# Performance work log

Measured on AMD Instinct MI355X. Metric: run time of the kernel, lower is better.

## Reference

```python
import jax, jax.numpy as jnp
import numpy as np

D_MODEL = 1024
NUM_HEADS = 16
D_K = D_MODEL // NUM_HEADS


def setup_inputs() -> dict:
    key = jax.random.key(0)
    ks = jax.random.split(key, 9)
    B, S = 4, 2048
    s = 1.0 / np.sqrt(D_MODEL)
    return {
        "x": jax.random.normal(ks[0], (B, S, D_MODEL), dtype=jnp.float32),
        "Wq": jax.random.uniform(ks[1], (D_MODEL, D_MODEL), jnp.float32, -s, s),
        "bq": jax.random.uniform(ks[2], (D_MODEL,), jnp.float32, -s, s),
        "Wk": jax.random.uniform(ks[3], (D_MODEL, D_MODEL), jnp.float32, -s, s),
        "bk": jax.random.uniform(ks[4], (D_MODEL,), jnp.float32, -s, s),
        "Wv": jax.random.uniform(ks[5], (D_MODEL, D_MODEL), jnp.float32, -s, s),
        "bv": jax.random.uniform(ks[6], (D_MODEL,), jnp.float32, -s, s),
        "Wo": jax.random.uniform(ks[7], (D_MODEL, D_MODEL), jnp.float32, -s, s),
        "bo": jax.random.uniform(ks[8], (D_MODEL,), jnp.float32, -s, s),
    }


def reference(x, Wq, bq, Wk, bk, Wv, bv, Wo, bo):
    B, S, D = x.shape
    H, dk = NUM_HEADS, D_K

    def proj(W, b):
        # [B,S,D] -> [B,H,S,dk]  (torch Linear: x @ W^T + b)
        y = jnp.einsum('bsd,ed->bse', x, W) + b
        return y.reshape(B, S, H, dk).transpose(0, 2, 1, 3)

    Q = proj(Wq, bq)
    K = proj(Wk, bk)
    V = proj(Wv, bv)

    scale = 1.0 / jnp.sqrt(jnp.asarray(dk, x.dtype))
    scores = jnp.einsum('bhqd,bhkd->bhqk', Q, K) * scale  # [B,H,S,S]
    attn = jax.nn.softmax(scores, axis=-1)
    # dropout is identity in eval mode
    out = jnp.einsum('bhqk,bhkd->bhqd', attn, V)  # [B,H,S,dk]
    out = out.transpose(0, 2, 1, 3).reshape(B, S, D)
    return jnp.einsum('bsd,ed->bse', out, Wo) + bo
```

## Files before the change

kernel.cpp:

```cpp
#include <hip/hip_runtime.h>


typedef unsigned short u16;
typedef unsigned int u32;
typedef __attribute__((ext_vector_type(8))) short bf16x8;
typedef __attribute__((ext_vector_type(4))) float f32x4;
typedef __attribute__((ext_vector_type(4))) unsigned short u16x4;
typedef __attribute__((ext_vector_type(8))) unsigned short u16x8;

#define SEQ    2048
#define DMODEL 1024
#define NHEAD  16
#define DK     64
#define BATCH  4
#define MROWS  (BATCH * SEQ)
#define LCF    0.18033688011112042f

__device__ __forceinline__ u16 f2bf(float f) {
  unsigned int u = __float_as_uint(f);
  u += 0x7fffu + ((u >> 16) & 1u);
  return (u16)(u >> 16);
}

__device__ __forceinline__ void gload_lds16(const void* g, void* l) {
  __builtin_amdgcn_global_load_lds((const __attribute__((address_space(1))) void*)g,
                                   (__attribute__((address_space(3))) void*)l,
                                   16, 0, 0);
}

__global__ __launch_bounds__(256) void cvt_all(const float* __restrict__ x,
                                               const float* __restrict__ w0,
                                               const float* __restrict__ w1,
                                               const float* __restrict__ w2,
                                               const float* __restrict__ w3,
                                               u16* xb, u16* o0, u16* o1, u16* o2, u16* o3) {
  const int NX4 = MROWS * DMODEL / 4;
  int i = blockIdx.x * 256 + threadIdx.x;
  const float* src; u16* dst; int off;
  if (i < NX4) { src = x; dst = xb; off = i; }
  else {
    int j = i - NX4;
    int wi = j >> 18; off = j & 0x3FFFF;
    src = wi == 0 ? w0 : wi == 1 ? w1 : wi == 2 ? w2 : w3;
    dst = wi == 0 ? o0 : wi == 1 ? o1 : wi == 2 ? o2 : o3;
  }
  float4 v = ((const float4*)src)[off];
  u16x4 o;
  o.x = f2bf(v.x); o.y = f2bf(v.y); o.z = f2bf(v.z); o.w = f2bf(v.w);
  ((u16x4*)dst)[off] = o;
}

__global__ __launch_bounds__(256) void vtrans(const u16* __restrict__ vb,
                                              u16* __restrict__ vt) {
  __shared__ u16 T[64 * 80];
  const int t = threadIdx.x;
  const int st = blockIdx.x;
  const int bh = blockIdx.y;
  const int b = bh >> 4, h = bh & 15;
  const size_t ibase = (size_t)b * SEQ * DMODEL + h * DK + (size_t)st * 64 * DMODEL;
#pragma unroll
  for (int i = 0; i < 2; ++i) {
    const int r = (t >> 3) + i * 32, c = (t & 7) * 8;
    *(bf16x8*)&T[r * 80 + c] = *(const bf16x8*)(vb + ibase + (size_t)r * DMODEL + c);
  }
  __syncthreads();
  const int d = t >> 2, k0 = (t & 3) * 16;
  const size_t obase = (((size_t)bh) * DK + d) * SEQ + st * 64 + k0;
  u16x8 a, bv;
#pragma unroll
  for (int j = 0; j < 8; ++j) a[j]  = T[(k0 + j) * 80 + d];
#pragma unroll
  for (int j = 0; j < 8; ++j) bv[j] = T[(k0 + 8 + j) * 80 + d];
  *(u16x8*)(vt + obase)     = a;
  *(u16x8*)(vt + obase + 8) = bv;
}

template <int OUT_BF16>
__device__ __forceinline__ void gemm_body(const u16* __restrict__ A,
                                          const u16* __restrict__ Bw,
                                          const float* __restrict__ bias,
                                          void* __restrict__ outp,
                                          int bm, int bn, int M, int N, int K,
                                          float scale, u16* As, u16* Bs) {
  const int t = threadIdx.x, w = t >> 6, l = t & 63;
  const int wr = (w >> 1) * 64, wc = (w & 1) * 64;
  const int lrow = l & 15, kgrp = l >> 4;
  const int r_in = l >> 3;
  const int c_in = ((l & 7) ^ r_in) * 8;
  const int sw = lrow & 7;

  f32x4 acc[4][4] = {};

  for (int kt = 0; kt < K; kt += 64) {
#pragma unroll
    for (int it = 0; it < 4; ++it) {
      const int chunk = w * 4 + it;
      const int row = chunk * 8 + r_in;
      gload_lds16(A  + (size_t)(bm * 128 + row) * K + kt + c_in, (char*)As + chunk * 1024);
      gload_lds16(Bw + (size_t)(bn * 128 + row) * K + kt + c_in, (char*)Bs + chunk * 1024);
    }
    __syncthreads();
#pragma unroll
    for (int kc = 0; kc < 2; ++kc) {
      bf16x8 af[4], bfr[4];
      const int slot = (kc * 4 + kgrp) ^ sw;
#pragma unroll
      for (int m = 0; m < 4; ++m)
        af[m] = *(const bf16x8*)&As[(wr + m * 16 + lrow) * 64 + slot * 8];
#pragma unroll
      for (int n = 0; n < 4; ++n)
        bfr[n] = *(const bf16x8*)&Bs[(wc + n * 16 + lrow) * 64 + slot * 8];
#pragma unroll
      for (int m = 0; m < 4; ++m)
#pragma unroll
        for (int n = 0; n < 4; ++n)
          acc[m][n] = __builtin_amdgcn_mfma_f32_16x16x32_bf16(af[m], bfr[n], acc[m][n], 0, 0, 0);
    }
    __syncthreads();
  }

  const int cr0 = bm * 128 + wr, cc0 = bn * 128 + wc;
#pragma unroll
  for (int n = 0; n < 4; ++n) {
    const int col = cc0 + n * 16 + lrow;
    const float bv = bias[col];
#pragma unroll
    for (int m = 0; m < 4; ++m) {
#pragma unroll
      for (int r = 0; r < 4; ++r) {
        const int row = cr0 + m * 16 + kgrp * 4 + r;
        const float v = (acc[m][n][r] + bv) * scale;
        if (OUT_BF16) ((u16*)outp)[(size_t)row * N + col] = f2bf(v);
        else          ((float*)outp)[(size_t)row * N + col] = v;
      }
    }
  }
}

__global__ __launch_bounds__(256) void gemm_bt_f32(const u16* __restrict__ A,
                                                   const u16* __restrict__ Bw,
                                                   const float* __restrict__ bias,
                                                   float* __restrict__ outp,
                                                   int M, int N, int K) {
  __shared__ u16 As[128 * 64];
  __shared__ u16 Bs[128 * 64];
  gemm_body<0>(A, Bw, bias, outp, blockIdx.x, blockIdx.y, M, N, K, 1.0f, As, Bs);
}

__global__ __launch_bounds__(256) void gemm_qkv(const u16* __restrict__ A,
                                                const u16* __restrict__ W0,
                                                const u16* __restrict__ W1,
                                                const u16* __restrict__ W2,
                                                const float* __restrict__ b0,
                                                const float* __restrict__ b1,
                                                const float* __restrict__ b2,
                                                u16* o0, u16* o1, u16* o2) {
  __shared__ u16 As[128 * 64];
  __shared__ u16 Bs[128 * 64];
  const int sel = blockIdx.y >> 3, bn = blockIdx.y & 7;
  const u16* Bw = sel == 0 ? W0 : sel == 1 ? W1 : W2;
  const float* bias = sel == 0 ? b0 : sel == 1 ? b1 : b2;
  u16* outp = sel == 0 ? o0 : sel == 1 ? o1 : o2;
  const float scale = sel == 0 ? LCF : 1.0f;
  gemm_body<1>(A, Bw, bias, outp, blockIdx.x, bn, MROWS, DMODEL, DMODEL, scale, As, Bs);
}

__global__ __launch_bounds__(256, 4) void attn_kernel(const u16* __restrict__ Qg,
                                                      const u16* __restrict__ Kg,
                                                      const u16* __restrict__ Vt,
                                                      u16* __restrict__ Og) {
  __shared__ u16 Ks[2][64 * 64];
  __shared__ u16 Vs[2][64 * 64];

  const int t = threadIdx.x, w = t >> 6, l = t & 63;
  const int lrow = l & 15, kgrp = l >> 4;
  const int sw = lrow & 7;

  const int id = blockIdx.x;
  const int swzid = (id & 7) * 128 + (id >> 3);
  const int qt = swzid & 15, bh = swzid >> 4;
  const int b = bh >> 4, h = bh & 15;
  const size_t base  = (size_t)b * SEQ * DMODEL + h * DK;
  const size_t vbase = (size_t)bh * DK * SEQ;
  const int r_in = l >> 3;
  const int c_in = ((l & 7) ^ r_in) * 8;

  int kro[2];
#pragma unroll
  for (int it = 0; it < 2; ++it) {
    const int p = (w * 2 + it) * 8 + r_in;
    const int n_ = p >> 4, g_ = (p >> 2) & 3, rr = p & 3;
    kro[it] = (n_ >> 1) * 32 + g_ * 8 + (n_ & 1) * 4 + rr;
  }

  const int qr = qt * 128 + w * 32;
  bf16x8 aq[2][2];
#pragma unroll
  for (int rg = 0; rg < 2; ++rg) {
    const u16* qp = Qg + base + (size_t)(qr + rg * 16 + lrow) * DMODEL + kgrp * 8;
    aq[rg][0] = *(const bf16x8*)qp;
    aq[rg][1] = *(const bf16x8*)(qp + 32);
  }

  f32x4 o_acc[2][4] = {};
  float lsum[2] = {};

#define STAGE(kt_, buf_)                                                        \
  {                                                                             \
    const int k0_ = (kt_) * 64;                                                 \
    _Pragma("unroll")                                                           \
    for (int it = 0; it < 2; ++it) {                                            \
      const int chunk = w * 2 + it;                                             \
      const int r = chunk * 8 + r_in;                                           \
      gload_lds16(Kg + base + (size_t)(k0_ + kro[it]) * DMODEL + c_in,          \
                  (char*)&Ks[buf_][0] + chunk * 1024);                          \
      gload_lds16(Vt + vbase + (size_t)r * SEQ + k0_ + c_in,                    \
                  (char*)&Vs[buf_][0] + chunk * 1024);                          \
    }                                                                           \
  }

  STAGE(0, 0);

  for (int kt = 0; kt < SEQ / 64; ++kt) {
    const int buf = kt & 1;
    __syncthreads();
    if (kt + 1 < SEQ / 64) STAGE(kt + 1, buf ^ 1);

    f32x4 sc[2][4] = {};
    __builtin_amdgcn_s_setprio(1);
#pragma unroll
    for (int kc = 0; kc < 2; ++kc) {
      const int slot = (kc * 4 + kgrp) ^ sw;
#pragma unroll
      for (int n = 0; n < 4; ++n) {
        bf16x8 bk = *(const bf16x8*)&Ks[buf][(n * 16 + lrow) * 64 + slot * 8];
        sc[0][n] = __builtin_amdgcn_mfma_f32_16x16x32_bf16(bk, aq[0][kc], sc[0][n], 0, 0, 0);
        sc[1][n] = __builtin_amdgcn_mfma_f32_16x16x32_bf16(bk, aq[1][kc], sc[1][n], 0, 0, 0);
      }
    }
    __builtin_amdgcn_s_setprio(0);

    bf16x8 pa[2][2];
#pragma unroll
    for (int rg = 0; rg < 2; ++rg) {
      u32 pk[4][2];
      float lp = 0.0f;
#pragma unroll
      for (int n = 0; n < 4; ++n) {
        const float p0 = __builtin_amdgcn_exp2f(sc[rg][n][0]);
        const float p1 = __builtin_amdgcn_exp2f(sc[rg][n][1]);
        const float p2 = __builtin_amdgcn_exp2f(sc[rg][n][2]);
        const float p3 = __builtin_amdgcn_exp2f(sc[rg][n][3]);
        lp += (p0 + p1) + (p2 + p3);
        asm("v_cvt_pk_bf16_f32 %0, %1, %2" : "=v"(pk[n][0]) : "v"(p0), "v"(p1));
        asm("v_cvt_pk_bf16_f32 %0, %1, %2" : "=v"(pk[n][1]) : "v"(p2), "v"(p3));
      }
      lsum[rg] += lp;
      union { u32 u[4]; bf16x8 v; } f0, f1;
      f0.u[0] = pk[0][0]; f0.u[1] = pk[0][1]; f0.u[2] = pk[1][0]; f0.u[3] = pk[1][1];
      f1.u[0] = pk[2][0]; f1.u[1] = pk[2][1]; f1.u[2] = pk[3][0]; f1.u[3] = pk[3][1];
      pa[rg][0] = f0.v;
      pa[rg][1] = f1.v;
    }

    __builtin_amdgcn_s_setprio(1);
#pragma unroll
    for (int kc = 0; kc < 2; ++kc) {
      const int slot = (kc * 4 + kgrp) ^ sw;
#pragma unroll
      for (int n = 0; n < 4; ++n) {
        bf16x8 bv = *(const bf16x8*)&Vs[buf][(n * 16 + lrow) * 64 + slot * 8];
        o_acc[0][n] = __builtin_amdgcn_mfma_f32_16x16x32_bf16(pa[0][kc], bv, o_acc[0][n], 0, 0, 0);
        o_acc[1][n] = __builtin_amdgcn_mfma_f32_16x16x32_bf16(pa[1][kc], bv, o_acc[1][n], 0, 0, 0);
      }
    }
    __builtin_amdgcn_s_setprio(0);
  }
#undef STAGE

#pragma unroll
  for (int rg = 0; rg < 2; ++rg) {
    float Lq = lsum[rg];
    Lq += __shfl_xor(Lq, 16);
    Lq += __shfl_xor(Lq, 32);
#pragma unroll
    for (int r = 0; r < 4; ++r) {
      const float inv = 1.0f / __shfl(Lq, kgrp * 4 + r);
      const int row = qr + rg * 16 + kgrp * 4 + r;
#pragma unroll
      for (int n = 0; n < 4; ++n)
        Og[base + (size_t)row * DMODEL + n * 16 + lrow] = f2bf(o_acc[rg][n][r] * inv);
    }
  }
}

extern "C" void kernel_launch(void* const* d_in, const int* in_sizes, int n_in,
                              void* d_out, int out_size, void* d_ws, size_t ws_size,
                              hipStream_t stream) {
  const float* x  = (const float*)d_in[0];
  const float* Wq = (const float*)d_in[1];
  const float* bq = (const float*)d_in[2];
  const float* Wk = (const float*)d_in[3];
  const float* bk = (const float*)d_in[4];
  const float* Wv = (const float*)d_in[5];
  const float* bv = (const float*)d_in[6];
  const float* Wo = (const float*)d_in[7];
  const float* bo = (const float*)d_in[8];
  float* out = (float*)d_out;

  const size_t XB   = (size_t)MROWS * DMODEL * 2;
  const size_t WB   = (size_t)DMODEL * DMODEL * 2;
  const size_t NEED = XB * 5 + WB * 4;
  if (ws_size < NEED) return;

  char* ws = (char*)d_ws;
  u16* xb  = (u16*)(ws);
  u16* wqb = (u16*)(ws + XB);
  u16* wkb = (u16*)(ws + XB + WB);
  u16* wvb = (u16*)(ws + XB + 2 * WB);
  u16* wob = (u16*)(ws + XB + 3 * WB);
  u16* qb  = (u16*)(ws + XB + 4 * WB);
  u16* kb  = (u16*)(ws + 2 * XB + 4 * WB);
  u16* vb  = (u16*)(ws + 3 * XB + 4 * WB);
  u16* ab  = (u16*)(ws + 4 * XB + 4 * WB);
  u16* vt  = xb;

  const int NCVT = (MROWS * DMODEL / 4) + DMODEL * DMODEL;
  cvt_all<<<NCVT / 256, 256, 0, stream>>>(x, Wq, Wk, Wv, Wo, xb, wqb, wkb, wvb, wob);

  gemm_qkv<<<dim3(MROWS / 128, 24), 256, 0, stream>>>(xb, wqb, wkb, wvb,
                                                      bq, bk, bv, qb, kb, vb);

  vtrans<<<dim3(SEQ / 64, BATCH * NHEAD), 256, 0, stream>>>(vb, vt);

  attn_kernel<<<dim3(1024), 256, 0, stream>>>(qb, kb, vt, ab);

  gemm_bt_f32<<<dim3(MROWS / 128, DMODEL / 128), 256, 0, stream>>>(
      ab, wob, bo, out, MROWS, DMODEL, DMODEL);
}
```

Before: 182.5 us.

## Fuse V transpose into QKV GEMM epilogue and remap blocks across XCDs

```diff
diff --git a/kernel.cpp b/kernel.cpp
--- a/kernel.cpp
+++ b/kernel.cpp
@@ -50,38 +50,14 @@
   ((u16x4*)dst)[off] = o;
 }
 
-__global__ __launch_bounds__(256) void vtrans(const u16* __restrict__ vb,
-                                              u16* __restrict__ vt) {
-  __shared__ u16 T[64 * 80];
-  const int t = threadIdx.x;
-  const int st = blockIdx.x;
-  const int bh = blockIdx.y;
-  const int b = bh >> 4, h = bh & 15;
-  const size_t ibase = (size_t)b * SEQ * DMODEL + h * DK + (size_t)st * 64 * DMODEL;
-#pragma unroll
-  for (int i = 0; i < 2; ++i) {
-    const int r = (t >> 3) + i * 32, c = (t & 7) * 8;
-    *(bf16x8*)&T[r * 80 + c] = *(const bf16x8*)(vb + ibase + (size_t)r * DMODEL + c);
-  }
-  __syncthreads();
-  const int d = t >> 2, k0 = (t & 3) * 16;
-  const size_t obase = (((size_t)bh) * DK + d) * SEQ + st * 64 + k0;
-  u16x8 a, bv;
-#pragma unroll
-  for (int j = 0; j < 8; ++j) a[j]  = T[(k0 + j) * 80 + d];
-#pragma unroll
-  for (int j = 0; j < 8; ++j) bv[j] = T[(k0 + 8 + j) * 80 + d];
-  *(u16x8*)(vt + obase)     = a;
-  *(u16x8*)(vt + obase + 8) = bv;
-}
-
-template <int OUT_BF16>
+template <int OUT_F32>
 __device__ __forceinline__ void gemm_body(const u16* __restrict__ A,
                                           const u16* __restrict__ Bw,
                                           const float* __restrict__ bias,
                                           void* __restrict__ outp,
                                           int bm, int bn, int M, int N, int K,
-                                          float scale, u16* As, u16* Bs) {
+                                          float scale, int vt_mode,
+                                          u16* As, u16* Bs) {
   const int t = threadIdx.x, w = t >> 6, l = t & 63;
   const int wr = (w >> 1) * 64, wc = (w & 1) * 64;
   const int lrow = l & 15, kgrp = l >> 4;
@@ -120,6 +96,23 @@
   }
 
   const int cr0 = bm * 128 + wr, cc0 = bn * 128 + wc;
+  if (!OUT_F32 && vt_mode) {
+    const int s0 = (bm & 15) * 128 + wr + kgrp * 4;
+    u16* vtp = (u16*)outp + (size_t)(bm >> 4) * 1024 * 2048;
+#pragma unroll
+    for (int n = 0; n < 4; ++n) {
+      const int col = cc0 + n * 16 + lrow;
+      const float bv = bias[col];
+#pragma unroll
+      for (int m = 0; m < 4; ++m) {
+        u16x4 pk;
+#pragma unroll
+        for (int r = 0; r < 4; ++r) pk[r] = f2bf(acc[m][n][r] + bv);
+        *(u16x4*)&vtp[(size_t)col * 2048 + s0 + m * 16] = pk;
+      }
+    }
+    return;
+  }
 #pragma unroll
   for (int n = 0; n < 4; ++n) {
     const int col = cc0 + n * 16 + lrow;
@@ -130,8 +123,8 @@
       for (int r = 0; r < 4; ++r) {
         const int row = cr0 + m * 16 + kgrp * 4 + r;
         const float v = (acc[m][n][r] + bv) * scale;
-        if (OUT_BF16) ((u16*)outp)[(size_t)row * N + col] = f2bf(v);
-        else          ((float*)outp)[(size_t)row * N + col] = v;
+        if (OUT_F32) ((float*)outp)[(size_t)row * N + col] = v;
+        else         ((u16*)outp)[(size_t)row * N + col] = f2bf(v);
       }
     }
   }
@@ -140,11 +133,14 @@
 __global__ __launch_bounds__(256) void gemm_bt_f32(const u16* __restrict__ A,
                                                    const u16* __restrict__ Bw,
                                                    const float* __restrict__ bias,
-                                                   float* __restrict__ outp,
-                                                   int M, int N, int K) {
+                                                   float* __restrict__ outp) {
   __shared__ u16 As[128 * 64];
   __shared__ u16 Bs[128 * 64];
-  gemm_body<0>(A, Bw, bias, outp, blockIdx.x, blockIdx.y, M, N, K, 1.0f, As, Bs);
+  const int wg = blockIdx.x;
+  const int xcd = wg & 7, local = wg >> 3;
+  const int lm = local & 7, bn = local >> 3;
+  const int bm = xcd * 8 + lm;
+  gemm_body<1>(A, Bw, bias, outp, bm, bn, MROWS, DMODEL, DMODEL, 1.0f, 0, As, Bs);
 }
 
 __global__ __launch_bounds__(256) void gemm_qkv(const u16* __restrict__ A,
@@ -154,15 +150,20 @@
                                                 const float* __restrict__ b0,
                                                 const float* __restrict__ b1,
                                                 const float* __restrict__ b2,
-                                                u16* o0, u16* o1, u16* o2) {
+                                                u16* o0, u16* o1, u16* vt) {
   __shared__ u16 As[128 * 64];
   __shared__ u16 Bs[128 * 64];
-  const int sel = blockIdx.y >> 3, bn = blockIdx.y & 7;
+  const int wg = blockIdx.x;
+  const int xcd = wg & 7, local = wg >> 3;
+  const int lm = local & 7, lnsel = local >> 3;
+  const int bm = xcd * 8 + lm;
+  const int sel = lnsel >> 3, bn = lnsel & 7;
   const u16* Bw = sel == 0 ? W0 : sel == 1 ? W1 : W2;
   const float* bias = sel == 0 ? b0 : sel == 1 ? b1 : b2;
-  u16* outp = sel == 0 ? o0 : sel == 1 ? o1 : o2;
+  u16* outp = sel == 0 ? o0 : sel == 1 ? o1 : vt;
   const float scale = sel == 0 ? LCF : 1.0f;
-  gemm_body<1>(A, Bw, bias, outp, blockIdx.x, bn, MROWS, DMODEL, DMODEL, scale, As, Bs);
+  gemm_body<0>(A, Bw, bias, outp, bm, bn, MROWS, DMODEL, DMODEL, scale,
+               sel == 2 ? 1 : 0, As, Bs);
 }
 
 __global__ __launch_bounds__(256, 4) void attn_kernel(const u16* __restrict__ Qg,
@@ -321,20 +322,16 @@
   u16* wob = (u16*)(ws + XB + 3 * WB);
   u16* qb  = (u16*)(ws + XB + 4 * WB);
   u16* kb  = (u16*)(ws + 2 * XB + 4 * WB);
-  u16* vb  = (u16*)(ws + 3 * XB + 4 * WB);
+  u16* vt  = (u16*)(ws + 3 * XB + 4 * WB);
   u16* ab  = (u16*)(ws + 4 * XB + 4 * WB);
-  u16* vt  = xb;
 
   const int NCVT = (MROWS * DMODEL / 4) + DMODEL * DMODEL;
   cvt_all<<<NCVT / 256, 256, 0, stream>>>(x, Wq, Wk, Wv, Wo, xb, wqb, wkb, wvb, wob);
 
-  gemm_qkv<<<dim3(MROWS / 128, 24), 256, 0, stream>>>(xb, wqb, wkb, wvb,
-                                                      bq, bk, bv, qb, kb, vb);
-
-  vtrans<<<dim3(SEQ / 64, BATCH * NHEAD), 256, 0, stream>>>(vb, vt);
+  gemm_qkv<<<dim3(1536), 256, 0, stream>>>(xb, wqb, wkb, wvb,
+                                           bq, bk, bv, qb, kb, vt);
 
   attn_kernel<<<dim3(1024), 256, 0, stream>>>(qb, kb, vt, ab);
 
-  gemm_bt_f32<<<dim3(MROWS / 128, DMODEL / 128), 256, 0, stream>>>(
-      ab, wob, bo, out, MROWS, DMODEL, DMODEL);
-}
+  gemm_bt_f32<<<dim3(512), 256, 0, stream>>>(ab, wob, bo, out);
+}
```

Result: faster. 175.2 us, median of 2 (-4.0%).
